# Kernel optimization log

Measured on AMD Instinct MI355X. Metric: run time of the kernel, lower is better.

## Reference

```python
import jax, jax.numpy as jnp
import numpy as np

N_NODES = 50000


def gcn_conv(x, row, col, W, b):
    """PyG GCNConv: add self-loops, symmetric deg^-1/2 normalization,
    linear transform, scatter-add aggregation, bias.
    Self-loop contribution is added analytically (norm = dinv[i]^2)
    instead of appending edges."""
    n = x.shape[0]
    h = x @ W  # [N, out]
    # degree over edges-with-self-loops, counted at target (col)
    deg = jnp.zeros((n,), dtype=x.dtype).at[col].add(1.0) + 1.0
    dinv = jax.lax.rsqrt(deg)  # deg >= 1 thanks to self-loops
    norm = dinv[row] * dinv[col]  # [E]
    # neighbor aggregation: out[col] += norm * h[row]
    agg = jnp.zeros_like(h).at[col].add(norm[:, None] * h[row])
    # self-loop term: dinv[i]^2 * h[i]
    agg = agg + (dinv * dinv)[:, None] * h
    return agg + b


def setup_inputs() -> dict:
    key = jax.random.key(0)
    ks = jax.random.split(key, 8)
    d_in, d_hid, d_out = 128, 128, 128
    n_edges = 625000
    x = jax.random.normal(ks[0], (N_NODES, d_in), dtype=jnp.float32)
    edge_index = jax.random.randint(ks[1], (2, n_edges), 0, N_NODES, dtype=jnp.int64)
    # Glorot-style weights, zero bias (PyG GCNConv defaults)
    def glorot(k, fan_in, fan_out):
        s = jnp.sqrt(6.0 / (fan_in + fan_out)).astype(jnp.float32)
        return jax.random.uniform(k, (fan_in, fan_out), dtype=jnp.float32, minval=-s, maxval=s)
    return {
        "x": x,
        "edge_index": edge_index,
        "W1": glorot(ks[2], d_in, d_hid), "b1": jnp.zeros((d_hid,), jnp.float32),
        "W2": glorot(ks[3], d_hid, d_hid), "b2": jnp.zeros((d_hid,), jnp.float32),
        "W3": glorot(ks[4], d_hid, d_out), "b3": jnp.zeros((d_out,), jnp.float32),
    }


def reference(x, edge_index, W1, b1, W2, b2, W3, b3):
    row, col = edge_index[0], edge_index[1]
    h = jax.nn.relu(gcn_conv(x, row, col, W1, b1))
    h = jax.nn.relu(gcn_conv(h, row, col, W2, b2))
    out = gcn_conv(h, row, col, W3, b3)  # no ReLU on last layer
    return out
```

## Files before the change

### kernel.cpp

```cpp
#include <hip/hip_runtime.h>
#include <hip/hip_fp16.h>

#define NN 50000
#define NE 625000
#define D 128
#define SCAN_BLK 1024
#define NSB ((NN + SCAN_BLK - 1) / SCAN_BLK)

typedef _Float16 half8 __attribute__((ext_vector_type(8)));
typedef float f32x4 __attribute__((ext_vector_type(4)));

union H8U4 { _Float16 h[8]; uint4 u; };


__global__ void zero_kernel(int4* __restrict__ p) {
    int i = blockIdx.x * blockDim.x + threadIdx.x;
    if (i < NN / 4 + 1) p[i] = make_int4(0, 0, 0, 0);
}

__global__ void count_kernel(const int* __restrict__ col, int* __restrict__ counts) {
    int i = blockIdx.x * blockDim.x + threadIdx.x;
    if (i < NE) atomicAdd(&counts[col[i]], 1);
}

__global__ __launch_bounds__(256) void scan1_kernel(const int* __restrict__ counts,
                                                    int* __restrict__ excl,
                                                    int* __restrict__ blocksums) {
    const int b = blockIdx.x, t = threadIdx.x;
    const int base = b * SCAN_BLK + t * 4;
    int v0 = 0, v1 = 0, v2 = 0, v3 = 0;
    if (base + 3 < NN) {
        int4 c = *(const int4*)(counts + base);
        v0 = c.x; v1 = c.y; v2 = c.z; v3 = c.w;
    } else {
        if (base     < NN) v0 = counts[base];
        if (base + 1 < NN) v1 = counts[base + 1];
        if (base + 2 < NN) v2 = counts[base + 2];
        if (base + 3 < NN) v3 = counts[base + 3];
    }
    const int s = v0 + v1 + v2 + v3;
    const int lane = t & 63, wid = t >> 6;
    int inc = s;
    #pragma unroll
    for (int off = 1; off < 64; off <<= 1) {
        int n = __shfl_up(inc, off, 64);
        if (lane >= off) inc += n;
    }
    __shared__ int wsum[4];
    if (lane == 63) wsum[wid] = inc;
    __syncthreads();
    int wbase = 0;
    for (int w = 0; w < wid; w++) wbase += wsum[w];
    const int texcl = wbase + inc - s;
    if (base     < NN) excl[base]     = texcl;
    if (base + 1 < NN) excl[base + 1] = texcl + v0;
    if (base + 2 < NN) excl[base + 2] = texcl + v0 + v1;
    if (base + 3 < NN) excl[base + 3] = texcl + v0 + v1 + v2;
    if (t == 255) blocksums[b] = wbase + inc;
}

__global__ __launch_bounds__(64) void scan2_kernel(const int* __restrict__ blocksums,
                                                   int* __restrict__ blockoff) {
    const int t = threadIdx.x;
    int v = (t < NSB) ? blocksums[t] : 0;
    int inc = v;
    #pragma unroll
    for (int off = 1; off < 64; off <<= 1) {
        int n = __shfl_up(inc, off, 64);
        if (t >= off) inc += n;
    }
    if (t < NSB) blockoff[t] = inc - v;
}

__global__ void scan3_kernel(const int* __restrict__ counts, const int* __restrict__ excl,
                             const int* __restrict__ blockoff, int* __restrict__ offsets,
                             int* __restrict__ cursor, float* __restrict__ dinv) {
    const int i = blockIdx.x * blockDim.x + threadIdx.x;
    if (i < NN) {
        const int o = excl[i] + blockoff[i >> 10];
        offsets[i] = o;
        cursor[i] = o;
        dinv[i] = rsqrtf((float)counts[i] + 1.0f);
    }
    if (i == 0) offsets[NN] = NE;
}

__global__ void fill_kernel(const int* __restrict__ row, const int* __restrict__ col,
                            const float* __restrict__ dinv, int* __restrict__ cursor,
                            uint32_t* __restrict__ csr) {
    int i = blockIdx.x * blockDim.x + threadIdx.x;
    if (i < NE) {
        int r = row[i], c = col[i];
        int p = atomicAdd(&cursor[c], 1);
        __half hw = __float2half_rn(dinv[r] * dinv[c]);
        csr[p] = (uint32_t)r | ((uint32_t)*(const unsigned short*)&hw << 16);
    }
}


__global__ __launch_bounds__(256) void wpack_kernel(const float* __restrict__ W,
                                                    uint4* __restrict__ wp) {
    int t = blockIdx.x * blockDim.x + threadIdx.x;
    if (t >= 2048) return;
    int lane = t & 63, entry = t >> 6;
    int ks = entry >> 3, ctg = entry & 7;
    int j = ctg * 16 + (lane & 15);
    int kb = ks * 32 + (lane >> 4) * 8;
    H8U4 u;
    #pragma unroll
    for (int e = 0; e < 8; e++) u.h[e] = (_Float16)W[(kb + e) * 128 + j];
    wp[t] = u.u;
}


template <bool IN_F16>
__global__ __launch_bounds__(256) void gemm_mfma(const void* __restrict__ Ain,
                                                 const uint4* __restrict__ wpack,
                                                 uint32_t* __restrict__ Hh) {
    __shared__ alignas(16) _Float16 Cs[64][152];
    const int t = threadIdx.x;
    const int w = t >> 6, l = t & 63;
    const int row0 = blockIdx.x * 64;
    const int lr = l & 15;
    const int lg = l >> 4;

    int arow[4];
    #pragma unroll
    for (int rt = 0; rt < 4; rt++) {
        int gr = row0 + rt * 16 + lr;
        arow[rt] = (gr < NN) ? gr : NN - 1;
    }

    f32x4 acc[4][2];
    #pragma unroll
    for (int rt = 0; rt < 4; rt++)
        #pragma unroll
        for (int ct = 0; ct < 2; ct++)
            acc[rt][ct] = (f32x4){0.f, 0.f, 0.f, 0.f};

    #pragma unroll
    for (int ks = 0; ks < 4; ks++) {
        const int kbase = ks * 32 + lg * 8;
        half8 af[4];
        if (IN_F16) {
            const uint4* A = (const uint4*)Ain;
            #pragma unroll
            for (int rt = 0; rt < 4; rt++) {
                H8U4 u;
                u.u = A[arow[rt] * 16 + (kbase >> 3)];
                af[rt] = *(half8*)u.h;
            }
        } else {
            const float4* A = (const float4*)Ain;
            #pragma unroll
            for (int rt = 0; rt < 4; rt++) {
                float4 p0 = A[arow[rt] * 32 + (kbase >> 2)];
                float4 p1 = A[arow[rt] * 32 + (kbase >> 2) + 1];
                half8 h;
                h[0] = (_Float16)p0.x; h[1] = (_Float16)p0.y;
                h[2] = (_Float16)p0.z; h[3] = (_Float16)p0.w;
                h[4] = (_Float16)p1.x; h[5] = (_Float16)p1.y;
                h[6] = (_Float16)p1.z; h[7] = (_Float16)p1.w;
                af[rt] = h;
            }
        }
        half8 bf[2];
        #pragma unroll
        for (int ct = 0; ct < 2; ct++) {
            H8U4 u;
            u.u = wpack[(ks * 8 + (w * 2 + ct)) * 64 + l];
            bf[ct] = *(half8*)u.h;
        }
        #pragma unroll
        for (int rt = 0; rt < 4; rt++)
            #pragma unroll
            for (int ct = 0; ct < 2; ct++)
                acc[rt][ct] = __builtin_amdgcn_mfma_f32_16x16x32_f16(
                    af[rt], bf[ct], acc[rt][ct], 0, 0, 0);
    }

    #pragma unroll
    for (int rt = 0; rt < 4; rt++)
        #pragma unroll
        for (int ct = 0; ct < 2; ct++) {
            const int col = w * 32 + ct * 16 + lr;
            #pragma unroll
            for (int r = 0; r < 4; r++)
                Cs[rt * 16 + lg * 4 + r][col] = (_Float16)acc[rt][ct][r];
        }
    __syncthreads();

    #pragma unroll
    for (int i = t; i < 1024; i += 256) {
        const int row = i >> 4, c16 = i & 15;
        if (row0 + row < NN) {
            uint4 u = *(const uint4*)&Cs[row][c16 * 8];
            *(uint4*)(Hh + (size_t)(row0 + row) * 64 + c16 * 4) = u;
        }
    }
}


static __device__ __forceinline__ void proc_edge(uint32_t rec, bool valid, int lh,
                                                 const uint2* __restrict__ hh2,
                                                 float4& acc) {
    const int s = (int)(rec & 0xffffu);
    unsigned short wb = (unsigned short)(rec >> 16);
    float w = valid ? __half2float(*(const __half*)&wb) : 0.0f;
    uint2 v = hh2[(size_t)s * 32 + lh];
    float2 lo = __half22float2(*(const __half2*)&v.x);
    float2 hi = __half22float2(*(const __half2*)&v.y);
    acc.x += w * lo.x;
    acc.y += w * lo.y;
    acc.z += w * hi.x;
    acc.w += w * hi.y;
}

template <bool OUT_F16>
__global__ __launch_bounds__(256) void agg_kernel(const uint2* __restrict__ hh2,
                                                  const int* __restrict__ offsets,
                                                  const uint32_t* __restrict__ csr,
                                                  const float* __restrict__ dinv,
                                                  const float* __restrict__ bias,
                                                  void* __restrict__ out,
                                                  const int relu) {
    const int node = blockIdx.x * 4 + (threadIdx.x >> 6);
    if (node >= NN) return;
    const int l = threadIdx.x & 63;
    const int half = l >> 5, lh = l & 31;
    const float di = dinv[node];
    const float sw = di * di;
    const int e0 = offsets[node];
    const int e1 = offsets[node + 1];

    float4 acc0 = make_float4(0.f, 0.f, 0.f, 0.f);
    float4 acc1 = make_float4(0.f, 0.f, 0.f, 0.f);
    float4 acc2 = make_float4(0.f, 0.f, 0.f, 0.f);
    float4 acc3 = make_float4(0.f, 0.f, 0.f, 0.f);

    if (e0 < e1) {
        const int elast = e1 - 1;
        uint32_t r0 = csr[min(e0 + 0 + half, elast)];
        uint32_t r1 = csr[min(e0 + 2 + half, elast)];
        uint32_t r2 = csr[min(e0 + 4 + half, elast)];
        uint32_t r3 = csr[min(e0 + 6 + half, elast)];
        for (int eb = e0; eb < e1; eb += 8) {
            const int nb = eb + 8;
            uint32_t n0 = csr[min(nb + 0 + half, elast)];
            uint32_t n1 = csr[min(nb + 2 + half, elast)];
            uint32_t n2 = csr[min(nb + 4 + half, elast)];
            uint32_t n3 = csr[min(nb + 6 + half, elast)];
            proc_edge(r0, eb + 0 + half < e1, lh, hh2, acc0);
            proc_edge(r1, eb + 2 + half < e1, lh, hh2, acc1);
            proc_edge(r2, eb + 4 + half < e1, lh, hh2, acc2);
            proc_edge(r3, eb + 6 + half < e1, lh, hh2, acc3);
            r0 = n0; r1 = n1; r2 = n2; r3 = n3;
        }
    }

    float4 s;
    s.x = (acc0.x + acc1.x) + (acc2.x + acc3.x);
    s.y = (acc0.y + acc1.y) + (acc2.y + acc3.y);
    s.z = (acc0.z + acc1.z) + (acc2.z + acc3.z);
    s.w = (acc0.w + acc1.w) + (acc2.w + acc3.w);
    s.x += __shfl_xor(s.x, 32, 64);
    s.y += __shfl_xor(s.y, 32, 64);
    s.z += __shfl_xor(s.z, 32, 64);
    s.w += __shfl_xor(s.w, 32, 64);

    uint2 sv = hh2[(size_t)node * 32 + lh];
    float2 slo = __half22float2(*(const __half2*)&sv.x);
    float2 shi = __half22float2(*(const __half2*)&sv.y);
    float4 bv = ((const float4*)bias)[lh];
    s.x += sw * slo.x + bv.x;
    s.y += sw * slo.y + bv.y;
    s.z += sw * shi.x + bv.z;
    s.w += sw * shi.y + bv.w;
    if (relu) {
        s.x = fmaxf(s.x, 0.f);
        s.y = fmaxf(s.y, 0.f);
        s.z = fmaxf(s.z, 0.f);
        s.w = fmaxf(s.w, 0.f);
    }
    if (half == 0) {
        if (OUT_F16) {
            __half2 p0 = __float22half2_rn(make_float2(s.x, s.y));
            __half2 p1 = __float22half2_rn(make_float2(s.z, s.w));
            uint2 u = make_uint2(*(const uint32_t*)&p0, *(const uint32_t*)&p1);
            *(uint2*)((uint32_t*)out + (size_t)node * 64 + lh * 2) = u;
        } else {
            ((float4*)out)[(size_t)node * 32 + lh] = s;
        }
    }
}


extern "C" void kernel_launch(void* const* d_in, const int* in_sizes, int n_in,
                              void* d_out, int out_size, void* d_ws, size_t ws_size,
                              hipStream_t stream) {
    (void)in_sizes; (void)n_in; (void)out_size; (void)ws_size;
    const float* x  = (const float*)d_in[0];
    const int*   ei = (const int*)d_in[1];
    const float* W1 = (const float*)d_in[2];
    const float* b1 = (const float*)d_in[3];
    const float* W2 = (const float*)d_in[4];
    const float* b2 = (const float*)d_in[5];
    const float* W3 = (const float*)d_in[6];
    const float* b3 = (const float*)d_in[7];
    const int* row = ei;
    const int* col = ei + NE;
    float* outp = (float*)d_out;

    char* ws = (char*)d_ws;
    size_t off = 0;
    auto walloc = [&](size_t bytes) -> void* {
        void* p = ws + off;
        off = (off + bytes + 255) & ~(size_t)255;
        return p;
    };
    int*      counts   = (int*)walloc(NN * 4 + 16);
    int*      excl     = (int*)walloc(NN * 4);
    int*      blocksums= (int*)walloc(NSB * 4);
    int*      blockoff = (int*)walloc(NSB * 4);
    int*      offsets  = (int*)walloc((NN + 1) * 4);
    int*      cursor   = (int*)walloc(NN * 4);
    float*    dinv     = (float*)walloc(NN * 4);
    uint32_t* csr      = (uint32_t*)walloc((size_t)NE * 4);
    uint32_t* act16    = (uint32_t*)walloc((size_t)NN * D * 2);
    uint32_t* hh16     = (uint32_t*)walloc((size_t)NN * D * 2);
    uint4*    wp1      = (uint4*)walloc(2048 * 16);
    uint4*    wp2      = (uint4*)walloc(2048 * 16);
    uint4*    wp3      = (uint4*)walloc(2048 * 16);

    zero_kernel<<<(NN / 4 + 1 + 255) / 256, 256, 0, stream>>>((int4*)counts);
    count_kernel<<<(NE + 255) / 256, 256, 0, stream>>>(col, counts);
    scan1_kernel<<<NSB, 256, 0, stream>>>(counts, excl, blocksums);
    scan2_kernel<<<1, 64, 0, stream>>>(blocksums, blockoff);
    scan3_kernel<<<(NN + 255) / 256, 256, 0, stream>>>(counts, excl, blockoff,
                                                       offsets, cursor, dinv);
    fill_kernel<<<(NE + 255) / 256, 256, 0, stream>>>(row, col, dinv, cursor, csr);
    wpack_kernel<<<8, 256, 0, stream>>>(W1, wp1);
    wpack_kernel<<<8, 256, 0, stream>>>(W2, wp2);
    wpack_kernel<<<8, 256, 0, stream>>>(W3, wp3);

    const int gblocks = (NN + 63) / 64;
    const int ablocks = (NN + 3) / 4;
    const uint2* hh2 = (const uint2*)hh16;
    gemm_mfma<false><<<gblocks, 256, 0, stream>>>(x, wp1, hh16);
    agg_kernel<true><<<ablocks, 256, 0, stream>>>(hh2, offsets, csr, dinv, b1, act16, 1);
    gemm_mfma<true><<<gblocks, 256, 0, stream>>>(act16, wp2, hh16);
    agg_kernel<true><<<ablocks, 256, 0, stream>>>(hh2, offsets, csr, dinv, b2, act16, 1);
    gemm_mfma<true><<<gblocks, 256, 0, stream>>>(act16, wp3, hh16);
    agg_kernel<false><<<ablocks, 256, 0, stream>>>(hh2, offsets, csr, dinv, b3, outp, 0);
}
```

Measured before the change: 215.8 us.

## Widen aggregation gathers to 16-byte loads, fuse scan and weight-pack kernels

The aggregation kernel now has 16 lanes each gather a 16-byte chunk of a neighbor row, so one wave covers 4 edges per load step instead of 2 and uses fewer, wider memory requests. Partial sums are then combined with two cross-lane shuffles. The three-kernel prefix scan is replaced by one single-block 1024-thread scan, and the three weight-pack launches are merged into one, cutting launch count. The single-block scan is serial per thread over 49 elements, which may cost latency, and the 16-lane layout raises register use per thread.

```diff
diff --git a/kernel.cpp b/kernel.cpp
--- a/kernel.cpp
+++ b/kernel.cpp
@@ -4,8 +4,7 @@
 #define NN 50000
 #define NE 625000
 #define D 128
-#define SCAN_BLK 1024
-#define NSB ((NN + SCAN_BLK - 1) / SCAN_BLK)
+#define CPT 49
 
 typedef _Float16 half8 __attribute__((ext_vector_type(8)));
 typedef float f32x4 __attribute__((ext_vector_type(4)));
@@ -23,66 +22,51 @@
     if (i < NE) atomicAdd(&counts[col[i]], 1);
 }
 
-__global__ __launch_bounds__(256) void scan1_kernel(const int* __restrict__ counts,
-                                                    int* __restrict__ excl,
-                                                    int* __restrict__ blocksums) {
-    const int b = blockIdx.x, t = threadIdx.x;
-    const int base = b * SCAN_BLK + t * 4;
-    int v0 = 0, v1 = 0, v2 = 0, v3 = 0;
-    if (base + 3 < NN) {
-        int4 c = *(const int4*)(counts + base);
-        v0 = c.x; v1 = c.y; v2 = c.z; v3 = c.w;
-    } else {
-        if (base     < NN) v0 = counts[base];
-        if (base + 1 < NN) v1 = counts[base + 1];
-        if (base + 2 < NN) v2 = counts[base + 2];
-        if (base + 3 < NN) v3 = counts[base + 3];
-    }
-    const int s = v0 + v1 + v2 + v3;
+__global__ __launch_bounds__(1024) void scan_all(const int* __restrict__ counts,
+                                                 int* __restrict__ offsets,
+                                                 int* __restrict__ cursor,
+                                                 float* __restrict__ dinv) {
+    const int t = threadIdx.x;
+    const int base = t * CPT;
+    int sum = 0;
+    for (int i = 0; i < CPT; i++) {
+        int idx = base + i;
+        if (idx < NN) sum += counts[idx];
+    }
     const int lane = t & 63, wid = t >> 6;
-    int inc = s;
+    int inc = sum;
     #pragma unroll
     for (int off = 1; off < 64; off <<= 1) {
         int n = __shfl_up(inc, off, 64);
         if (lane >= off) inc += n;
     }
-    __shared__ int wsum[4];
+    __shared__ int wsum[16];
+    __shared__ int woff[16];
     if (lane == 63) wsum[wid] = inc;
     __syncthreads();
-    int wbase = 0;
-    for (int w = 0; w < wid; w++) wbase += wsum[w];
-    const int texcl = wbase + inc - s;
-    if (base     < NN) excl[base]     = texcl;
-    if (base + 1 < NN) excl[base + 1] = texcl + v0;
-    if (base + 2 < NN) excl[base + 2] = texcl + v0 + v1;
-    if (base + 3 < NN) excl[base + 3] = texcl + v0 + v1 + v2;
-    if (t == 255) blocksums[b] = wbase + inc;
-}
-
-__global__ __launch_bounds__(64) void scan2_kernel(const int* __restrict__ blocksums,
-                                                   int* __restrict__ blockoff) {
-    const int t = threadIdx.x;
-    int v = (t < NSB) ? blocksums[t] : 0;
-    int inc = v;
-    #pragma unroll
-    for (int off = 1; off < 64; off <<= 1) {
-        int n = __shfl_up(inc, off, 64);
-        if (t >= off) inc += n;
-    }
-    if (t < NSB) blockoff[t] = inc - v;
-}
-
-__global__ void scan3_kernel(const int* __restrict__ counts, const int* __restrict__ excl,
-                             const int* __restrict__ blockoff, int* __restrict__ offsets,
-                             int* __restrict__ cursor, float* __restrict__ dinv) {
-    const int i = blockIdx.x * blockDim.x + threadIdx.x;
-    if (i < NN) {
-        const int o = excl[i] + blockoff[i >> 10];
-        offsets[i] = o;
-        cursor[i] = o;
-        dinv[i] = rsqrtf((float)counts[i] + 1.0f);
-    }
-    if (i == 0) offsets[NN] = NE;
+    if (t < 16) {
+        int v = wsum[t];
+        int winc = v;
+        #pragma unroll
+        for (int off = 1; off < 16; off <<= 1) {
+            int n = __shfl_up(winc, off, 16);
+            if (t >= off) winc += n;
+        }
+        woff[t] = winc - v;
+    }
+    __syncthreads();
+    int running = woff[wid] + (inc - sum);
+    for (int i = 0; i < CPT; i++) {
+        int idx = base + i;
+        if (idx < NN) {
+            int v = counts[idx];
+            offsets[idx] = running;
+            cursor[idx] = running;
+            dinv[idx] = rsqrtf((float)v + 1.0f);
+            running += v;
+        }
+    }
+    if (t == 0) offsets[NN] = NE;
 }
 
 __global__ void fill_kernel(const int* __restrict__ row, const int* __restrict__ col,
@@ -98,10 +82,14 @@
 }
 
 
-__global__ __launch_bounds__(256) void wpack_kernel(const float* __restrict__ W,
-                                                    uint4* __restrict__ wp) {
-    int t = blockIdx.x * blockDim.x + threadIdx.x;
-    if (t >= 2048) return;
+__global__ __launch_bounds__(256) void wpack3_kernel(const float* __restrict__ W1,
+                                                     const float* __restrict__ W2,
+                                                     const float* __restrict__ W3,
+                                                     uint4* __restrict__ wp) {
+    const int b = blockIdx.x;
+    const float* W = (b < 8) ? W1 : (b < 16) ? W2 : W3;
+    uint4* dst = wp + (size_t)(b >> 3) * 2048;
+    int t = (b & 7) * 256 + threadIdx.x;
     int lane = t & 63, entry = t >> 6;
     int ks = entry >> 3, ctg = entry & 7;
     int j = ctg * 16 + (lane & 15);
@@ -109,7 +97,7 @@
     H8U4 u;
     #pragma unroll
     for (int e = 0; e < 8; e++) u.h[e] = (_Float16)W[(kb + e) * 128 + j];
-    wp[t] = u.u;
+    dst[t] = u.u;
 }
 
 
@@ -201,23 +189,25 @@
 }
 
 
-static __device__ __forceinline__ void proc_edge(uint32_t rec, bool valid, int lh,
-                                                 const uint2* __restrict__ hh2,
-                                                 float4& acc) {
+static __device__ __forceinline__ void proc4(uint32_t rec, bool valid, int lg,
+                                             const uint4* __restrict__ hh4,
+                                             float* __restrict__ acc) {
     const int s = (int)(rec & 0xffffu);
     unsigned short wb = (unsigned short)(rec >> 16);
-    float w = valid ? __half2float(*(const __half*)&wb) : 0.0f;
-    uint2 v = hh2[(size_t)s * 32 + lh];
-    float2 lo = __half22float2(*(const __half2*)&v.x);
-    float2 hi = __half22float2(*(const __half2*)&v.y);
-    acc.x += w * lo.x;
-    acc.y += w * lo.y;
-    acc.z += w * hi.x;
-    acc.w += w * hi.y;
+    const float w = valid ? __half2float(*(const __half*)&wb) : 0.0f;
+    uint4 v = hh4[(size_t)s * 16 + lg];
+    float2 f0 = __half22float2(*(const __half2*)&v.x);
+    float2 f1 = __half22float2(*(const __half2*)&v.y);
+    float2 f2 = __half22float2(*(const __half2*)&v.z);
+    float2 f3 = __half22float2(*(const __half2*)&v.w);
+    acc[0] += w * f0.x; acc[1] += w * f0.y;
+    acc[2] += w * f1.x; acc[3] += w * f1.y;
+    acc[4] += w * f2.x; acc[5] += w * f2.y;
+    acc[6] += w * f3.x; acc[7] += w * f3.y;
 }
 
 template <bool OUT_F16>
-__global__ __launch_bounds__(256) void agg_kernel(const uint2* __restrict__ hh2,
+__global__ __launch_bounds__(256) void agg_kernel(const uint4* __restrict__ hh4,
                                                   const int* __restrict__ offsets,
                                                   const uint32_t* __restrict__ csr,
                                                   const float* __restrict__ dinv,
@@ -227,69 +217,71 @@
     const int node = blockIdx.x * 4 + (threadIdx.x >> 6);
     if (node >= NN) return;
     const int l = threadIdx.x & 63;
-    const int half = l >> 5, lh = l & 31;
+    const int g = l >> 4;
+    const int lg = l & 15;
     const float di = dinv[node];
     const float sw = di * di;
     const int e0 = offsets[node];
     const int e1 = offsets[node + 1];
 
-    float4 acc0 = make_float4(0.f, 0.f, 0.f, 0.f);
-    float4 acc1 = make_float4(0.f, 0.f, 0.f, 0.f);
-    float4 acc2 = make_float4(0.f, 0.f, 0.f, 0.f);
-    float4 acc3 = make_float4(0.f, 0.f, 0.f, 0.f);
+    float a0[8], a1[8];
+    #pragma unroll
+    for (int i = 0; i < 8; i++) { a0[i] = 0.f; a1[i] = 0.f; }
 
     if (e0 < e1) {
         const int elast = e1 - 1;
-        uint32_t r0 = csr[min(e0 + 0 + half, elast)];
-        uint32_t r1 = csr[min(e0 + 2 + half, elast)];
-        uint32_t r2 = csr[min(e0 + 4 + half, elast)];
-        uint32_t r3 = csr[min(e0 + 6 + half, elast)];
+        uint32_t r0 = csr[min(e0 + g, elast)];
+        uint32_t r1 = csr[min(e0 + 4 + g, elast)];
         for (int eb = e0; eb < e1; eb += 8) {
             const int nb = eb + 8;
-            uint32_t n0 = csr[min(nb + 0 + half, elast)];
-            uint32_t n1 = csr[min(nb + 2 + half, elast)];
-            uint32_t n2 = csr[min(nb + 4 + half, elast)];
-            uint32_t n3 = csr[min(nb + 6 + half, elast)];
-            proc_edge(r0, eb + 0 + half < e1, lh, hh2, acc0);
-            proc_edge(r1, eb + 2 + half < e1, lh, hh2, acc1);
-            proc_edge(r2, eb + 4 + half < e1, lh, hh2, acc2);
-            proc_edge(r3, eb + 6 + half < e1, lh, hh2, acc3);
-            r0 = n0; r1 = n1; r2 = n2; r3 = n3;
-        }
-    }
-
-    float4 s;
-    s.x = (acc0.x + acc1.x) + (acc2.x + acc3.x);
-    s.y = (acc0.y + acc1.y) + (acc2.y + acc3.y);
-    s.z = (acc0.z + acc1.z) + (acc2.z + acc3.z);
-    s.w = (acc0.w + acc1.w) + (acc2.w + acc3.w);
-    s.x += __shfl_xor(s.x, 32, 64);
-    s.y += __shfl_xor(s.y, 32, 64);
-    s.z += __shfl_xor(s.z, 32, 64);
-    s.w += __shfl_xor(s.w, 32, 64);
-
-    uint2 sv = hh2[(size_t)node * 32 + lh];
-    float2 slo = __half22float2(*(const __half2*)&sv.x);
-    float2 shi = __half22float2(*(const __half2*)&sv.y);
-    float4 bv = ((const float4*)bias)[lh];
-    s.x += sw * slo.x + bv.x;
-    s.y += sw * slo.y + bv.y;
-    s.z += sw * shi.x + bv.z;
-    s.w += sw * shi.y + bv.w;
+            uint32_t n0 = csr[min(nb + g, elast)];
+            uint32_t n1 = csr[min(nb + 4 + g, elast)];
+            proc4(r0, eb + g < e1, lg, hh4, a0);
+            proc4(r1, eb + 4 + g < e1, lg, hh4, a1);
+            r0 = n0; r1 = n1;
+        }
+    }
+
+    float s[8];
+    #pragma unroll
+    for (int i = 0; i < 8; i++) s[i] = a0[i] + a1[i];
+    #pragma unroll
+    for (int i = 0; i < 8; i++) s[i] += __shfl_xor(s[i], 16, 64);
+    #pragma unroll
+    for (int i = 0; i < 8; i++) s[i] += __shfl_xor(s[i], 32, 64);
+
+    uint4 sv = hh4[(size_t)node * 16 + lg];
+    float2 f0 = __half22float2(*(const __half2*)&sv.x);
+    float2 f1 = __half22float2(*(const __half2*)&sv.y);
+    float2 f2 = __half22float2(*(const __half2*)&sv.z);
+    float2 f3 = __half22float2(*(const __half2*)&sv.w);
+    float4 b0 = ((const float4*)bias)[lg * 2];
+    float4 b1 = ((const float4*)bias)[lg * 2 + 1];
+    s[0] += sw * f0.x + b0.x; s[1] += sw * f0.y + b0.y;
+    s[2] += sw * f1.x + b0.z; s[3] += sw * f1.y + b0.w;
+    s[4] += sw * f2.x + b1.x; s[5] += sw * f2.y + b1.y;
+    s[6] += sw * f3.x + b1.z; s[7] += sw * f3.y + b1.w;
     if (relu) {
-        s.x = fmaxf(s.x, 0.f);
-        s.y = fmaxf(s.y, 0.f);
-        s.z = fmaxf(s.z, 0.f);
-        s.w = fmaxf(s.w, 0.f);
-    }
-    if (half == 0) {
+        #pragma unroll
+        for (int i = 0; i < 8; i++) s[i] = fmaxf(s[i], 0.f);
+    }
+    if (g == 0) {
         if (OUT_F16) {
-            __half2 p0 = __float22half2_rn(make_float2(s.x, s.y));
-            __half2 p1 = __float22half2_rn(make_float2(s.z, s.w));
-            uint2 u = make_uint2(*(const uint32_t*)&p0, *(const uint32_t*)&p1);
-            *(uint2*)((uint32_t*)out + (size_t)node * 64 + lh * 2) = u;
+            __half2 p0 = __float22half2_rn(make_float2(s[0], s[1]));
+            __half2 p1 = __float22half2_rn(make_float2(s[2], s[3]));
+            __half2 p2 = __float22half2_rn(make_float2(s[4], s[5]));
+            __half2 p3 = __float22half2_rn(make_float2(s[6], s[7]));
+            uint4 u;
+            u.x = *(const uint32_t*)&p0;
+            u.y = *(const uint32_t*)&p1;
+            u.z = *(const uint32_t*)&p2;
+            u.w = *(const uint32_t*)&p3;
+            ((uint4*)out)[(size_t)node * 16 + lg] = u;
         } else {
-            ((float4*)out)[(size_t)node * 32 + lh] = s;
+            float4 o0 = make_float4(s[0], s[1], s[2], s[3]);
+            float4 o1 = make_float4(s[4], s[5], s[6], s[7]);
+            ((float4*)out)[(size_t)node * 32 + lg * 2] = o0;
+            ((float4*)out)[(size_t)node * 32 + lg * 2 + 1] = o1;
         }
     }
 }
@@ -319,37 +311,27 @@
         return p;
     };
     int*      counts   = (int*)walloc(NN * 4 + 16);
-    int*      excl     = (int*)walloc(NN * 4);
-    int*      blocksums= (int*)walloc(NSB * 4);
-    int*      blockoff = (int*)walloc(NSB * 4);
     int*      offsets  = (int*)walloc((NN + 1) * 4);
     int*      cursor   = (int*)walloc(NN * 4);
     float*    dinv     = (float*)walloc(NN * 4);
     uint32_t* csr      = (uint32_t*)walloc((size_t)NE * 4);
     uint32_t* act16    = (uint32_t*)walloc((size_t)NN * D * 2);
     uint32_t* hh16     = (uint32_t*)walloc((size_t)NN * D * 2);
-    uint4*    wp1      = (uint4*)walloc(2048 * 16);
-    uint4*    wp2      = (uint4*)walloc(2048 * 16);
-    uint4*    wp3      = (uint4*)walloc(2048 * 16);
+    uint4*    wp       = (uint4*)walloc(3 * 2048 * 16);
 
     zero_kernel<<<(NN / 4 + 1 + 255) / 256, 256, 0, stream>>>((int4*)counts);
     count_kernel<<<(NE + 255) / 256, 256, 0, stream>>>(col, counts);
-    scan1_kernel<<<NSB, 256, 0, stream>>>(counts, excl, blocksums);
-    scan2_kernel<<<1, 64, 0, stream>>>(blocksums, blockoff);
-    scan3_kernel<<<(NN + 255) / 256, 256, 0, stream>>>(counts, excl, blockoff,
-                                                       offsets, cursor, dinv);
+    scan_all<<<1, 1024, 0, stream>>>(counts, offsets, cursor, dinv);
     fill_kernel<<<(NE + 255) / 256, 256, 0, stream>>>(row, col, dinv, cursor, csr);
-    wpack_kernel<<<8, 256, 0, stream>>>(W1, wp1);
-    wpack_kernel<<<8, 256, 0, stream>>>(W2, wp2);
-    wpack_kernel<<<8, 256, 0, stream>>>(W3, wp3);
+    wpack3_kernel<<<24, 256, 0, stream>>>(W1, W2, W3, wp);
 
     const int gblocks = (NN + 63) / 64;
     const int ablocks = (NN + 3) / 4;
-    const uint2* hh2 = (const uint2*)hh16;
-    gemm_mfma<false><<<gblocks, 256, 0, stream>>>(x, wp1, hh16);
-    agg_kernel<true><<<ablocks, 256, 0, stream>>>(hh2, offsets, csr, dinv, b1, act16, 1);
-    gemm_mfma<true><<<gblocks, 256, 0, stream>>>(act16, wp2, hh16);
-    agg_kernel<true><<<ablocks, 256, 0, stream>>>(hh2, offsets, csr, dinv, b2, act16, 1);
-    gemm_mfma<true><<<gblocks, 256, 0, stream>>>(act16, wp3, hh16);
-    agg_kernel<false><<<ablocks, 256, 0, stream>>>(hh2, offsets, csr, dinv, b3, outp, 0);
-}
+    const uint4* hh4 = (const uint4*)hh16;
+    gemm_mfma<false><<<gblocks, 256, 0, stream>>>(x, wp, hh16);
+    agg_kernel<true><<<ablocks, 256, 0, stream>>>(hh4, offsets, csr, dinv, b1, act16, 1);
+    gemm_mfma<true><<<gblocks, 256, 0, stream>>>(act16, wp + 2048, hh16);
+    agg_kernel<true><<<ablocks, 256, 0, stream>>>(hh4, offsets, csr, dinv, b2, act16, 1);
+    gemm_mfma<true><<<gblocks, 256, 0, stream>>>(act16, wp + 4096, hh16);
+    agg_kernel<false><<<ablocks, 256, 0, stream>>>(hh4, offsets, csr, dinv, b3, outp, 0);
+}
```

After: 349.3 us. +61.9%, slower.
